# Kernel tuning notes

Measured on AMD Instinct MI355X. Metric: run time of the kernel, lower is better.

## Reference

```python
import jax, jax.numpy as jnp
import numpy as np

DECAY = 0.2
THRESH = 0.5
LENS = 0.5
B, T, IN, HID, OUT = 128, 16, 2048, 2048, 1024  # OUT = 4*num_classes


@jax.custom_vjp
def act_fun(x):
    # spike = (mem > thresh).float() with surrogate gradient in bwd
    return (x > THRESH).astype(x.dtype)

def _act_fwd(x):
    return act_fun(x), x

def _act_bwd(x, g):
    return (g * (jnp.abs(x - THRESH) < LENS).astype(g.dtype),)

act_fun.defvjp(_act_fwd, _act_bwd)


def setup_inputs() -> dict:
    key = jax.random.key(0)
    ks = jax.random.split(key, 5)
    s1 = 1.0 / np.sqrt(IN)
    s2 = 1.0 / np.sqrt(HID)
    return {
        "x": jax.random.normal(ks[0], (B, T, IN), jnp.float32),
        "fc1_w": jax.random.uniform(ks[1], (HID, IN), jnp.float32, -s1, s1),
        "fc1_b": jax.random.uniform(ks[2], (HID,), jnp.float32, -s1, s1),
        "fc2_w": jax.random.uniform(ks[3], (OUT, HID), jnp.float32, -s2, s2),
        "fc2_b": jax.random.uniform(ks[4], (OUT,), jnp.float32, -s2, s2),
        "time_window": T,
    }


def reference(x, fc1_w, fc1_b, fc2_w, fc2_b, time_window):
    xt = jnp.swapaxes(x, 0, 1)  # [T, B, IN]
    b = x.shape[0]
    hid = fc1_w.shape[0]
    out = fc2_w.shape[0]

    def mem_update(w, bias, inp, mem, spike):
        mem = mem * DECAY * (1.0 - spike) + inp @ w.T + bias
        return mem, act_fun(mem)

    def inner(carry, x_t):
        h1m, h1s, h2m, h2s, acc = carry
        h1m, h1s = mem_update(fc1_w, fc1_b, x_t, h1m, h1s)
        h2m, h2s = mem_update(fc2_w, fc2_b, h1s, h2m, h2s)
        return (h1m, h1s, h2m, h2s, acc + h2s), None

    def outer(carry, _):
        h1m, h1s, h2m, h2s, _ = carry
        # sum_out resets each outer step; mem/spike state carries over
        acc0 = jnp.zeros((b, out), x.dtype)
        carry, _ = jax.lax.scan(inner, (h1m, h1s, h2m, h2s, acc0), xt)
        return carry, None

    z1 = jnp.zeros((b, hid), x.dtype)
    z2 = jnp.zeros((b, out), x.dtype)
    carry, _ = jax.lax.scan(outer, (z1, z1, z2, z2, z2), None, length=time_window)
    return carry[4]  # sum of h2 spikes over last outer iteration
```

## Files before the change

### kernel.cpp

```cpp
#include <hip/hip_runtime.h>
#include <hip/hip_bf16.h>

constexpr int B   = 128;
constexpr int T   = 16;
constexpr int IN  = 2048;
constexpr int HID = 2048;
constexpr int OUT = 1024;
constexpr int TAU = 256;
constexpr int CHUNK = 64;
constexpr float DECAY  = 0.2f;
constexpr float THRESH = 0.5f;

typedef short  v8s  __attribute__((ext_vector_type(8)));
typedef float  f32x4 __attribute__((ext_vector_type(4)));

__device__ __forceinline__ float bf2f(unsigned short u) {
    union { unsigned int i; float f; } v; v.i = ((unsigned int)u) << 16; return v.f;
}
__device__ __forceinline__ unsigned short f2bf_rne(float f) {
    union { float f; unsigned int i; } v; v.f = f;
    return (unsigned short)((v.i + 0x7FFFu + ((v.i >> 16) & 1u)) >> 16);
}

__device__ __forceinline__ void gload_lds16(const void* g, void* l) {
    __builtin_amdgcn_global_load_lds(
        (const __attribute__((address_space(1))) void*)g,
        (__attribute__((address_space(3))) void*)l, 16, 0, 0);
}

__global__ __launch_bounds__(256)
void wsplit(const float* __restrict__ W, unsigned short* __restrict__ Wh,
            unsigned short* __restrict__ Wm, unsigned short* __restrict__ Wl)
{
    int i = blockIdx.x * 256 + threadIdx.x;
    float4 w = *(const float4*)(W + (size_t)i * 4);
    float wv[4] = { w.x, w.y, w.z, w.w };
    unsigned short h[4], m[4], lo[4];
    #pragma unroll
    for (int j = 0; j < 4; j++) {
        h[j]  = f2bf_rne(wv[j]);  float r1 = wv[j] - bf2f(h[j]);
        m[j]  = f2bf_rne(r1);     float r2 = r1 - bf2f(m[j]);
        lo[j] = f2bf_rne(r2);
    }
    *(ushort4*)(Wh + (size_t)i * 4) = make_ushort4(h[0], h[1], h[2], h[3]);
    *(ushort4*)(Wm + (size_t)i * 4) = make_ushort4(m[0], m[1], m[2], m[3]);
    *(ushort4*)(Wl + (size_t)i * 4) = make_ushort4(lo[0], lo[1], lo[2], lo[3]);
}

__global__ __launch_bounds__(256, 4)
void gemm1_f32v2(const float* __restrict__ A, const float* __restrict__ W,
                 const float* __restrict__ bias, float* __restrict__ C,
                 int M, int N, int K)
{
    __shared__ float As[16][68];
    __shared__ float Bs[16][68];
    const int tid = threadIdx.x;
    const int tx = tid & 15, ty = tid >> 4;
    const int row0 = blockIdx.y * 64, col0 = blockIdx.x * 64;

    float acc[4][4];
    #pragma unroll
    for (int i = 0; i < 4; i++)
        #pragma unroll
        for (int j = 0; j < 4; j++) acc[i][j] = 0.f;

    const int sr = tid >> 2;
    const int sk = (tid & 3) << 2;

    for (int k0 = 0; k0 < K; k0 += 16) {
        float4 av = *(const float4*)(A + (size_t)(row0 + sr) * K + (k0 + sk));
        float4 bv = *(const float4*)(W + (size_t)(col0 + sr) * K + (k0 + sk));
        __syncthreads();
        As[sk + 0][sr] = av.x; As[sk + 1][sr] = av.y;
        As[sk + 2][sr] = av.z; As[sk + 3][sr] = av.w;
        Bs[sk + 0][sr] = bv.x; Bs[sk + 1][sr] = bv.y;
        Bs[sk + 2][sr] = bv.z; Bs[sk + 3][sr] = bv.w;
        __syncthreads();
        #pragma unroll
        for (int k = 0; k < 16; k++) {
            float4 a = *(const float4*)&As[k][ty * 4];
            float4 b = *(const float4*)&Bs[k][tx * 4];
            float ar[4] = { a.x, a.y, a.z, a.w };
            float br[4] = { b.x, b.y, b.z, b.w };
            #pragma unroll
            for (int i = 0; i < 4; i++)
                #pragma unroll
                for (int j = 0; j < 4; j++)
                    acc[i][j] = fmaf(ar[i], br[j], acc[i][j]);
        }
    }
    #pragma unroll
    for (int i = 0; i < 4; i++) {
        size_t r = (size_t)(row0 + ty * 4 + i);
        int c0 = col0 + tx * 4;
        float4 o;
        o.x = acc[i][0] + bias[c0 + 0];
        o.y = acc[i][1] + bias[c0 + 1];
        o.z = acc[i][2] + bias[c0 + 2];
        o.w = acc[i][3] + bias[c0 + 3];
        *(float4*)(C + r * N + c0) = o;
    }
}

__global__ __launch_bounds__(256)
void rec1(const float* __restrict__ Z1, unsigned long long* __restrict__ Sbits)
{
    int idx = blockIdx.x * 256 + threadIdx.x;
    int h = idx & (HID - 1);
    int b = idx >> 11;
    float z[16];
    #pragma unroll
    for (int t = 0; t < 16; t++)
        z[t] = Z1[((size_t)(b * T + t)) * HID + h];
    const size_t wbase = (size_t)b * (HID / 64) + (h >> 6);
    const bool lead = (threadIdx.x & 63) == 0;
    float m = 0.f, s = 0.f;
    for (int tau = 0; tau < TAU; ++tau) {
        m = m * DECAY * (1.f - s) + z[tau & 15];
        unsigned long long mask = __ballot(m > THRESH);
        s = (m > THRESH) ? 1.f : 0.f;
        if (lead)
            Sbits[(size_t)tau * (B * HID / 64) + wbase] = mask;
    }
}

__global__ __launch_bounds__(256)
void gemm2_mfma(const unsigned char* __restrict__ Sbytes,
                const unsigned short* __restrict__ W2h,
                const unsigned short* __restrict__ W2m,
                const unsigned short* __restrict__ W2l,
                const float* __restrict__ bias,
                float* __restrict__ C,
                int m0glob)
{
    __shared__ unsigned short As[4096];
    __shared__ unsigned short Bs[3][4096];
    const int tid = threadIdx.x;
    const int l  = tid & 63, w = tid >> 6;
    const int wr = w >> 1, wc = w & 1;
    const int lg = l >> 4, lr = l & 15;
    const int row0 = blockIdx.y * 128, col0 = blockIdx.x * 128;

    f32x4 acc[4][4];
    #pragma unroll
    for (int m = 0; m < 4; m++)
        #pragma unroll
        for (int n = 0; n < 4; n++) acc[m][n] = (f32x4){0.f, 0.f, 0.f, 0.f};

    const int g_a = tid >> 5, u = tid & 31;
    const int r_a = u & 15, s_lo = (u >> 4) << 1;
    const unsigned char* arow =
        Sbytes + (size_t)(m0glob + row0 + g_a * 16 + r_a) * 256 + s_lo;
    unsigned short* As_w0 = &As[(g_a * 64 + s_lo * 16 + r_a) * 8];
    unsigned short* As_w1 = &As[(g_a * 64 + (s_lo + 1) * 16 + r_a) * 8];

    const int s_b = (tid >> 4) & 3, r_b = tid & 15;
    const size_t boff1 = (size_t)(col0 + w * 16 + r_b) * 2048 + s_b * 8;
    const size_t boff2 = (size_t)(col0 + (w + 4) * 16 + r_b) * 2048 + s_b * 8;
    unsigned short* bdst1 = &Bs[0][w * 512];
    unsigned short* bdst2 = &Bs[0][2048 + w * 512];

    for (int k0 = 0; k0 < HID; k0 += 32) {
        unsigned int bits = *(const unsigned short*)(arow + (k0 >> 3));
        __syncthreads();
        gload_lds16(W2h + boff1 + k0, bdst1);
        gload_lds16(W2h + boff2 + k0, bdst2);
        gload_lds16(W2m + boff1 + k0, bdst1 + 4096);
        gload_lds16(W2m + boff2 + k0, bdst2 + 4096);
        gload_lds16(W2l + boff1 + k0, bdst1 + 8192);
        gload_lds16(W2l + boff2 + k0, bdst2 + 8192);
        unsigned int q[8];
        #pragma unroll
        for (int j = 0; j < 8; j++)
            q[j] = (((bits >> (2 * j)) & 1u) ? 0x3F80u : 0u) |
                   (((bits >> (2 * j + 1)) & 1u) ? 0x3F800000u : 0u);
        *(uint4*)As_w0 = make_uint4(q[0], q[1], q[2], q[3]);
        *(uint4*)As_w1 = make_uint4(q[4], q[5], q[6], q[7]);
        __syncthreads();

        v8s a[4];
        #pragma unroll
        for (int m = 0; m < 4; m++)
            a[m] = *(const v8s*)&As[(((wr * 4 + m) * 4 + lg) * 16 + lr) * 8];
        #pragma unroll
        for (int sp = 0; sp < 3; sp++) {
            #pragma unroll
            for (int n = 0; n < 4; n++) {
                v8s b = *(const v8s*)&Bs[sp][(((wc * 4 + n) * 4 + lg) * 16 + lr) * 8];
                #pragma unroll
                for (int m = 0; m < 4; m++)
                    acc[m][n] = __builtin_amdgcn_mfma_f32_16x16x32_bf16(
                                    a[m], b, acc[m][n], 0, 0, 0);
            }
        }
    }

    #pragma unroll
    for (int m = 0; m < 4; m++) {
        int row = row0 + wr * 64 + m * 16 + (lg << 2);
        #pragma unroll
        for (int n = 0; n < 4; n++) {
            int col = col0 + wc * 64 + n * 16 + lr;
            float bv = bias[col];
            #pragma unroll
            for (int q2 = 0; q2 < 4; q2++)
                C[(size_t)(row + q2) * OUT + col] = acc[m][n][q2] + bv;
        }
    }
}

__global__ __launch_bounds__(256)
void rec2_chunk(const float* __restrict__ Z2c, float* __restrict__ m_state,
                float* __restrict__ s_state, float* __restrict__ out,
                int tau0, int last)
{
    int idx = blockIdx.x * 256 + threadIdx.x;
    int o = idx & (OUT - 1);
    int b = idx >> 10;
    float m, s;
    if (tau0 == 0) { m = 0.f; s = 0.f; }
    else           { m = m_state[idx]; s = s_state[idx]; }
    float acc = 0.f;
    for (int tl = 0; tl < CHUNK; ++tl) {
        float zv = Z2c[((size_t)(tl * B + b)) * OUT + o];
        m = m * DECAY * (1.f - s) + zv;
        s = (m > THRESH) ? 1.f : 0.f;
        if (tau0 + tl >= TAU - 16) acc += s;
    }
    m_state[idx] = m;
    s_state[idx] = s;
    if (last) out[idx] = acc;
}

extern "C" void kernel_launch(void* const* d_in, const int* in_sizes, int n_in,
                              void* d_out, int out_size, void* d_ws, size_t ws_size,
                              hipStream_t stream)
{
    const float* x     = (const float*)d_in[0];
    const float* fc1_w = (const float*)d_in[1];
    const float* fc1_b = (const float*)d_in[2];
    const float* fc2_w = (const float*)d_in[3];
    const float* fc2_b = (const float*)d_in[4];
    float* out = (float*)d_out;

    char* ws = (char*)d_ws;
    float* Z1  = (float*)ws;
    float* Z2c = (float*)ws;
    unsigned long long* Sbits = (unsigned long long*)(ws + 33554432);
    unsigned short* W2h = (unsigned short*)(ws + 33554432 + 8388608);
    unsigned short* W2m = W2h + (size_t)OUT * HID;
    unsigned short* W2l = W2m + (size_t)OUT * HID;
    float* m_state = (float*)(ws + 33554432 + 8388608 + 3 * 4194304);
    float* s_state = m_state + B * OUT;

    wsplit<<<(OUT * HID / 4) / 256, 256, 0, stream>>>(fc2_w, W2h, W2m, W2l);

    {
        dim3 grid(HID / 64, (B * T) / 64);
        gemm1_f32v2<<<grid, 256, 0, stream>>>(x, fc1_w, fc1_b, Z1, B * T, HID, IN);
    }
    rec1<<<(B * HID) / 256, 256, 0, stream>>>(Z1, Sbits);

    const unsigned char* Sbytes = (const unsigned char*)Sbits;
    for (int c = 0; c < TAU / CHUNK; ++c) {
        dim3 grid(OUT / 128, (CHUNK * B) / 128);
        gemm2_mfma<<<grid, 256, 0, stream>>>(Sbytes, W2h, W2m, W2l, fc2_b, Z2c,
                                             c * CHUNK * B);
        rec2_chunk<<<(B * OUT) / 256, 256, 0, stream>>>(
            Z2c, m_state, s_state, out, c * CHUNK, (c == TAU / CHUNK - 1) ? 1 : 0);
    }
}
```

Before: 818.5 us.

## Replace 3-way bf16 split GEMM2 with 4-slice int8 MFMA and widen GEMM1 K tile

The fc2 weights are now stored as four int8 fixed-point slices instead of a three-way bf16 split. The binary spike matrix is multiplied against them with i32 16x16x64 int8 MFMAs in two passes, and each slice's integer accumulator is rescaled and summed into fp32. This aims to cut weight bytes and raise MFMA throughput while keeping near-fp32 accuracy, but it relies on |w|*32 < 1 and gives a different rounding profile. Separately, the fp32 GEMM1 loads a K tile of 32 per iteration instead of 16, which halves its barrier count.

```diff
diff --git a/kernel.cpp b/kernel.cpp
--- a/kernel.cpp
+++ b/kernel.cpp
@@ -11,16 +11,8 @@
 constexpr float DECAY  = 0.2f;
 constexpr float THRESH = 0.5f;
 
-typedef short  v8s  __attribute__((ext_vector_type(8)));
+typedef int    v4i   __attribute__((ext_vector_type(4)));
 typedef float  f32x4 __attribute__((ext_vector_type(4)));
-
-__device__ __forceinline__ float bf2f(unsigned short u) {
-    union { unsigned int i; float f; } v; v.i = ((unsigned int)u) << 16; return v.f;
-}
-__device__ __forceinline__ unsigned short f2bf_rne(float f) {
-    union { float f; unsigned int i; } v; v.f = f;
-    return (unsigned short)((v.i + 0x7FFFu + ((v.i >> 16) & 1u)) >> 16);
-}
 
 __device__ __forceinline__ void gload_lds16(const void* g, void* l) {
     __builtin_amdgcn_global_load_lds(
@@ -29,31 +21,39 @@
 }
 
 __global__ __launch_bounds__(256)
-void wsplit(const float* __restrict__ W, unsigned short* __restrict__ Wh,
-            unsigned short* __restrict__ Wm, unsigned short* __restrict__ Wl)
-{
+void wsplit_i8(const float* __restrict__ W, signed char* __restrict__ Q)
+{
+    const size_t SZ = (size_t)OUT * HID;
     int i = blockIdx.x * 256 + threadIdx.x;
     float4 w = *(const float4*)(W + (size_t)i * 4);
     float wv[4] = { w.x, w.y, w.z, w.w };
-    unsigned short h[4], m[4], lo[4];
+    signed char q[4][4];
     #pragma unroll
     for (int j = 0; j < 4; j++) {
-        h[j]  = f2bf_rne(wv[j]);  float r1 = wv[j] - bf2f(h[j]);
-        m[j]  = f2bf_rne(r1);     float r2 = r1 - bf2f(m[j]);
-        lo[j] = f2bf_rne(r2);
-    }
-    *(ushort4*)(Wh + (size_t)i * 4) = make_ushort4(h[0], h[1], h[2], h[3]);
-    *(ushort4*)(Wm + (size_t)i * 4) = make_ushort4(m[0], m[1], m[2], m[3]);
-    *(ushort4*)(Wl + (size_t)i * 4) = make_ushort4(lo[0], lo[1], lo[2], lo[3]);
+        float v = wv[j] * 32.0f;
+        float q0 = rintf(v * 128.f); v = v * 128.f - q0;
+        float q1 = rintf(v * 128.f); v = v * 128.f - q1;
+        float q2 = rintf(v * 128.f); v = v * 128.f - q2;
+        float q3 = rintf(v * 128.f);
+        q[0][j] = (signed char)(int)q0;
+        q[1][j] = (signed char)(int)q1;
+        q[2][j] = (signed char)(int)q2;
+        q[3][j] = (signed char)(int)q3;
+    }
+    #pragma unroll
+    for (int s = 0; s < 4; s++) {
+        char4 c; c.x = q[s][0]; c.y = q[s][1]; c.z = q[s][2]; c.w = q[s][3];
+        *(char4*)(Q + s * SZ + (size_t)i * 4) = c;
+    }
 }
 
 __global__ __launch_bounds__(256, 4)
-void gemm1_f32v2(const float* __restrict__ A, const float* __restrict__ W,
+void gemm1_f32v3(const float* __restrict__ A, const float* __restrict__ W,
                  const float* __restrict__ bias, float* __restrict__ C,
                  int M, int N, int K)
 {
-    __shared__ float As[16][68];
-    __shared__ float Bs[16][68];
+    __shared__ float As[32][68];
+    __shared__ float Bs[32][68];
     const int tid = threadIdx.x;
     const int tx = tid & 15, ty = tid >> 4;
     const int row0 = blockIdx.y * 64, col0 = blockIdx.x * 64;
@@ -64,20 +64,25 @@
         #pragma unroll
         for (int j = 0; j < 4; j++) acc[i][j] = 0.f;
 
-    const int sr = tid >> 2;
-    const int sk = (tid & 3) << 2;
-
-    for (int k0 = 0; k0 < K; k0 += 16) {
-        float4 av = *(const float4*)(A + (size_t)(row0 + sr) * K + (k0 + sk));
-        float4 bv = *(const float4*)(W + (size_t)(col0 + sr) * K + (k0 + sk));
+    const int sr = tid & 63;
+    const int kq = tid >> 6;
+
+    for (int k0 = 0; k0 < K; k0 += 32) {
+        const float* pa = A + (size_t)(row0 + sr) * K + k0 + kq * 8;
+        const float* pb = W + (size_t)(col0 + sr) * K + k0 + kq * 8;
+        float4 av0 = *(const float4*)pa, av1 = *(const float4*)(pa + 4);
+        float4 bv0 = *(const float4*)pb, bv1 = *(const float4*)(pb + 4);
         __syncthreads();
-        As[sk + 0][sr] = av.x; As[sk + 1][sr] = av.y;
-        As[sk + 2][sr] = av.z; As[sk + 3][sr] = av.w;
-        Bs[sk + 0][sr] = bv.x; Bs[sk + 1][sr] = bv.y;
-        Bs[sk + 2][sr] = bv.z; Bs[sk + 3][sr] = bv.w;
+        float avr[8] = { av0.x, av0.y, av0.z, av0.w, av1.x, av1.y, av1.z, av1.w };
+        float bvr[8] = { bv0.x, bv0.y, bv0.z, bv0.w, bv1.x, bv1.y, bv1.z, bv1.w };
+        #pragma unroll
+        for (int i = 0; i < 8; i++) {
+            As[kq * 8 + i][sr] = avr[i];
+            Bs[kq * 8 + i][sr] = bvr[i];
+        }
         __syncthreads();
         #pragma unroll
-        for (int k = 0; k < 16; k++) {
+        for (int k = 0; k < 32; k++) {
             float4 a = *(const float4*)&As[k][ty * 4];
             float4 b = *(const float4*)&Bs[k][tx * 4];
             float ar[4] = { a.x, a.y, a.z, a.w };
@@ -124,75 +129,104 @@
     }
 }
 
-__global__ __launch_bounds__(256)
-void gemm2_mfma(const unsigned char* __restrict__ Sbytes,
-                const unsigned short* __restrict__ W2h,
-                const unsigned short* __restrict__ W2m,
-                const unsigned short* __restrict__ W2l,
-                const float* __restrict__ bias,
-                float* __restrict__ C,
-                int m0glob)
-{
-    __shared__ unsigned short As[4096];
-    __shared__ unsigned short Bs[3][4096];
+__global__ __launch_bounds__(256, 2)
+void gemm2_i8(const unsigned char* __restrict__ Sbytes,
+              const signed char* __restrict__ W2q,
+              const float* __restrict__ bias,
+              float* __restrict__ C,
+              int m0glob)
+{
+    __shared__ unsigned char As8[8192];
+    __shared__ unsigned char Bs8[2][8192];
+    const size_t SZ = (size_t)OUT * HID;
     const int tid = threadIdx.x;
     const int l  = tid & 63, w = tid >> 6;
     const int wr = w >> 1, wc = w & 1;
     const int lg = l >> 4, lr = l & 15;
     const int row0 = blockIdx.y * 128, col0 = blockIdx.x * 128;
 
-    f32x4 acc[4][4];
+    f32x4 master[4][4];
     #pragma unroll
     for (int m = 0; m < 4; m++)
         #pragma unroll
-        for (int n = 0; n < 4; n++) acc[m][n] = (f32x4){0.f, 0.f, 0.f, 0.f};
-
-    const int g_a = tid >> 5, u = tid & 31;
-    const int r_a = u & 15, s_lo = (u >> 4) << 1;
-    const unsigned char* arow =
-        Sbytes + (size_t)(m0glob + row0 + g_a * 16 + r_a) * 256 + s_lo;
-    unsigned short* As_w0 = &As[(g_a * 64 + s_lo * 16 + r_a) * 8];
-    unsigned short* As_w1 = &As[(g_a * 64 + (s_lo + 1) * 16 + r_a) * 8];
-
-    const int s_b = (tid >> 4) & 3, r_b = tid & 15;
-    const size_t boff1 = (size_t)(col0 + w * 16 + r_b) * 2048 + s_b * 8;
-    const size_t boff2 = (size_t)(col0 + (w + 4) * 16 + r_b) * 2048 + s_b * 8;
-    unsigned short* bdst1 = &Bs[0][w * 512];
-    unsigned short* bdst2 = &Bs[0][2048 + w * 512];
-
-    for (int k0 = 0; k0 < HID; k0 += 32) {
-        unsigned int bits = *(const unsigned short*)(arow + (k0 >> 3));
-        __syncthreads();
-        gload_lds16(W2h + boff1 + k0, bdst1);
-        gload_lds16(W2h + boff2 + k0, bdst2);
-        gload_lds16(W2m + boff1 + k0, bdst1 + 4096);
-        gload_lds16(W2m + boff2 + k0, bdst2 + 4096);
-        gload_lds16(W2l + boff1 + k0, bdst1 + 8192);
-        gload_lds16(W2l + boff2 + k0, bdst2 + 8192);
-        unsigned int q[8];
-        #pragma unroll
-        for (int j = 0; j < 8; j++)
-            q[j] = (((bits >> (2 * j)) & 1u) ? 0x3F80u : 0u) |
-                   (((bits >> (2 * j + 1)) & 1u) ? 0x3F800000u : 0u);
-        *(uint4*)As_w0 = make_uint4(q[0], q[1], q[2], q[3]);
-        *(uint4*)As_w1 = make_uint4(q[4], q[5], q[6], q[7]);
-        __syncthreads();
-
-        v8s a[4];
+        for (int n = 0; n < 4; n++) master[m][n] = (f32x4){0.f, 0.f, 0.f, 0.f};
+
+    const int gA = tid >> 6, kgA = (tid >> 4) & 3, rA = tid & 15;
+    const size_t arow0 = (size_t)(m0glob + row0 + gA * 16 + rA) * 256 + kgA * 2;
+    const size_t arow1 = (size_t)(m0glob + row0 + (gA + 4) * 16 + rA) * 256 + kgA * 2;
+    unsigned char* aw0 = &As8[(size_t)tid * 16];
+    unsigned char* aw1 = &As8[(size_t)(tid + 256) * 16];
+
+    const int spl = w >> 1, sub = w & 1;
+    unsigned char* bbase = &Bs8[spl][0];
+    const int bcol = col0 + (l & 15);
+    const int bks  = ((l >> 4) & 3) * 16;
+
+    for (int pass = 0; pass < 2; ++pass) {
+        const signed char* wp = W2q + (size_t)(2 * pass + spl) * SZ;
+        v4i acc0[4][4], acc1[4][4];
         #pragma unroll
         for (int m = 0; m < 4; m++)
-            a[m] = *(const v8s*)&As[(((wr * 4 + m) * 4 + lg) * 16 + lr) * 8];
-        #pragma unroll
-        for (int sp = 0; sp < 3; sp++) {
             #pragma unroll
             for (int n = 0; n < 4; n++) {
-                v8s b = *(const v8s*)&Bs[sp][(((wc * 4 + n) * 4 + lg) * 16 + lr) * 8];
+                acc0[m][n] = (v4i){0, 0, 0, 0};
+                acc1[m][n] = (v4i){0, 0, 0, 0};
+            }
+
+        for (int k0 = 0; k0 < HID; k0 += 64) {
+            unsigned int bits0 = *(const unsigned short*)(Sbytes + arow0 + (k0 >> 3));
+            unsigned int bits1 = *(const unsigned short*)(Sbytes + arow1 + (k0 >> 3));
+            __syncthreads();
+            #pragma unroll
+            for (int iter = 0; iter < 4; iter++) {
+                int g = sub * 4 + iter;
+                gload_lds16(wp + (size_t)(bcol + g * 16) * 2048 + k0 + bks,
+                            bbase + (sub * 256 + iter * 64) * 16);
+            }
+            uint4 u0, u1;
+            {
+                unsigned int b0 = bits0, b1 = bits1;
+                u0.x = (((b0 >> 0)  & 0xFu) * 0x00204081u) & 0x01010101u;
+                u0.y = (((b0 >> 4)  & 0xFu) * 0x00204081u) & 0x01010101u;
+                u0.z = (((b0 >> 8)  & 0xFu) * 0x00204081u) & 0x01010101u;
+                u0.w = (((b0 >> 12) & 0xFu) * 0x00204081u) & 0x01010101u;
+                u1.x = (((b1 >> 0)  & 0xFu) * 0x00204081u) & 0x01010101u;
+                u1.y = (((b1 >> 4)  & 0xFu) * 0x00204081u) & 0x01010101u;
+                u1.z = (((b1 >> 8)  & 0xFu) * 0x00204081u) & 0x01010101u;
+                u1.w = (((b1 >> 12) & 0xFu) * 0x00204081u) & 0x01010101u;
+            }
+            *(uint4*)aw0 = u0;
+            *(uint4*)aw1 = u1;
+            __syncthreads();
+
+            v4i a[4];
+            #pragma unroll
+            for (int m = 0; m < 4; m++)
+                a[m] = *(const v4i*)&As8[(((wr * 4 + m) * 4 + lg) * 16 + lr) * 16];
+            #pragma unroll
+            for (int n = 0; n < 4; n++) {
+                v4i b0 = *(const v4i*)&Bs8[0][(((wc * 4 + n) * 4 + lg) * 16 + lr) * 16];
+                v4i b1 = *(const v4i*)&Bs8[1][(((wc * 4 + n) * 4 + lg) * 16 + lr) * 16];
                 #pragma unroll
-                for (int m = 0; m < 4; m++)
-                    acc[m][n] = __builtin_amdgcn_mfma_f32_16x16x32_bf16(
-                                    a[m], b, acc[m][n], 0, 0, 0);
+                for (int m = 0; m < 4; m++) {
+                    acc0[m][n] = __builtin_amdgcn_mfma_i32_16x16x64_i8(
+                                     a[m], b0, acc0[m][n], 0, 0, 0);
+                    acc1[m][n] = __builtin_amdgcn_mfma_i32_16x16x64_i8(
+                                     a[m], b1, acc1[m][n], 0, 0, 0);
+                }
             }
         }
+        const float sA = pass ? 0x1p-26f : 0x1p-12f;
+        const float sB = pass ? 0x1p-33f : 0x1p-19f;
+        #pragma unroll
+        for (int m = 0; m < 4; m++)
+            #pragma unroll
+            for (int n = 0; n < 4; n++)
+                #pragma unroll
+                for (int e = 0; e < 4; e++) {
+                    master[m][n][e] = fmaf(sA, (float)acc0[m][n][e], master[m][n][e]);
+                    master[m][n][e] = fmaf(sB, (float)acc1[m][n][e], master[m][n][e]);
+                }
     }
 
     #pragma unroll
@@ -204,7 +238,7 @@
             float bv = bias[col];
             #pragma unroll
             for (int q2 = 0; q2 < 4; q2++)
-                C[(size_t)(row + q2) * OUT + col] = acc[m][n][q2] + bv;
+                C[(size_t)(row + q2) * OUT + col] = master[m][n][q2] + bv;
         }
     }
 }
@@ -247,25 +281,23 @@
     float* Z1  = (float*)ws;
     float* Z2c = (float*)ws;
     unsigned long long* Sbits = (unsigned long long*)(ws + 33554432);
-    unsigned short* W2h = (unsigned short*)(ws + 33554432 + 8388608);
-    unsigned short* W2m = W2h + (size_t)OUT * HID;
-    unsigned short* W2l = W2m + (size_t)OUT * HID;
-    float* m_state = (float*)(ws + 33554432 + 8388608 + 3 * 4194304);
+    signed char* W2q = (signed char*)(ws + 33554432 + 8388608);
+    float* m_state = (float*)(ws + 33554432 + 8388608 + 4 * 2097152);
     float* s_state = m_state + B * OUT;
 
-    wsplit<<<(OUT * HID / 4) / 256, 256, 0, stream>>>(fc2_w, W2h, W2m, W2l);
+    wsplit_i8<<<(OUT * HID / 4) / 256, 256, 0, stream>>>(fc2_w, W2q);
 
     {
         dim3 grid(HID / 64, (B * T) / 64);
-        gemm1_f32v2<<<grid, 256, 0, stream>>>(x, fc1_w, fc1_b, Z1, B * T, HID, IN);
+        gemm1_f32v3<<<grid, 256, 0, stream>>>(x, fc1_w, fc1_b, Z1, B * T, HID, IN);
     }
     rec1<<<(B * HID) / 256, 256, 0, stream>>>(Z1, Sbits);
 
     const unsigned char* Sbytes = (const unsigned char*)Sbits;
     for (int c = 0; c < TAU / CHUNK; ++c) {
         dim3 grid(OUT / 128, (CHUNK * B) / 128);
-        gemm2_mfma<<<grid, 256, 0, stream>>>(Sbytes, W2h, W2m, W2l, fc2_b, Z2c,
-                                             c * CHUNK * B);
+        gemm2_i8<<<grid, 256, 0, stream>>>(Sbytes, W2q, fc2_b, Z2c,
+                                           c * CHUNK * B);
         rec2_chunk<<<(B * OUT) / 256, 256, 0, stream>>>(
             Z2c, m_state, s_state, out, c * CHUNK, (c == TAU / CHUNK - 1) ? 1 : 0);
     }
```

Result: slower. 868.6 us (+6.1%).
